# Kernel tuning notes

Hardware: AMD Instinct MI355X
Metric: run time of the kernel (lower is better)

Reference implementation:

```python
import jax, jax.numpy as jnp
import numpy as np


def _ctc_greedy_decode(probs, table, default_char):
    """Greedy CTC decode (tf.keras.backend.ctc_decode, greedy=True) + label->char lookup.

    probs: [B, T, C] post-softmax scores; blank index = C-1 (tf convention).
    Returns [B, T] int32 char codes, left-packed, padded positions -> default_char
    (tf pads the dense decoded tensor with -1; the hash-table lookup of -1 yields
    the table's default value).
    """
    B, T, C = probs.shape
    blank = C - 1
    best = jnp.argmax(probs, axis=-1).astype(jnp.int32)           # [B, T]
    # collapse repeats: keep first of each run
    prev = jnp.concatenate([jnp.full((B, 1), -1, jnp.int32), best[:, :-1]], axis=1)
    valid = (best != prev) & (best != blank)                      # [B, T]
    # left-pack valid labels via scatter (invalid entries routed to a dummy column T)
    pos = jnp.cumsum(valid.astype(jnp.int32), axis=1) - 1         # output slot per step
    scatter_col = jnp.where(valid, pos, T)
    out = jnp.full((B, T + 1), -1, jnp.int32)
    b_idx = jnp.arange(B)[:, None]
    out = out.at[b_idx, scatter_col].set(best)
    labels = out[:, :T]                                           # [B, T], -1 padded
    # hash-table lookup: valid labels -> chars, -1 padding -> default_value
    chars = jnp.where(labels >= 0,
                      table[jnp.clip(labels, 0, C - 1)],
                      jnp.int32(default_char))
    return chars


def setup_inputs() -> dict:
    key = jax.random.key(0)
    k1, k2 = jax.random.split(key)
    B, T, C = 1024, 512, 128
    inputs = jax.random.uniform(k1, (B, T, C), dtype=jnp.float32)
    table = jax.random.randint(k2, (C,), 0, 128, dtype=jnp.int32)
    return {"inputs": inputs, "table": table, "default_char": 32}


def reference(inputs, table, default_char):
    return _ctc_greedy_decode(inputs, table, default_char)
```

## Files before the change

### kernel.cpp

```cpp
#include <hip/hip_runtime.h>


constexpr int T_DIM = 512;
constexpr int C_DIM = 128;
constexpr int BLANK = C_DIM - 1;
constexpr int BLOCK = 512;
constexpr int TS_PER_ITER = BLOCK / 8;
constexpr int N_ITER = T_DIM / TS_PER_ITER;

__global__ __launch_bounds__(BLOCK, 4) void ctc_decode_kernel(
    const float* __restrict__ probs,
    const int* __restrict__ table,
    const int* __restrict__ defc_p,
    int* __restrict__ out)
{
    __shared__ int s_best[T_DIM];
    __shared__ int s_chars[T_DIM];
    __shared__ int s_table[C_DIM];
    __shared__ int s_wavesums[BLOCK / 64];

    const int b    = blockIdx.x;
    const int tid  = threadIdx.x;
    const int lane = tid & 63;
    const int wave = tid >> 6;

    if (tid < C_DIM) s_table[tid] = table[tid];
    const int defc = defc_p[0];

    const float* row = probs + (size_t)b * T_DIM * C_DIM;

    const int g = lane >> 3;
    const int h = lane & 7;

    float4 pf[4];
    {
        const float* p0 = row + (size_t)(wave * 8 + g) * C_DIM + h * 4;
        #pragma unroll
        for (int j = 0; j < 4; ++j) pf[j] = *(const float4*)(p0 + j * 32);
    }

    for (int it = 0; it < N_ITER; ++it) {
        float4 v[4];
        #pragma unroll
        for (int j = 0; j < 4; ++j) v[j] = pf[j];

        if (it + 1 < N_ITER) {
            const float* pn = row + (size_t)((it + 1) * TS_PER_ITER + wave * 8 + g) * C_DIM + h * 4;
            #pragma unroll
            for (int j = 0; j < 4; ++j) pf[j] = *(const float4*)(pn + j * 32);
        }

        float bv = -1.0f; int bi = 0;
        #pragma unroll
        for (int j = 0; j < 4; ++j) {
            const int i0 = j * 32 + h * 4;
            if (v[j].x > bv) { bv = v[j].x; bi = i0;     }
            if (v[j].y > bv) { bv = v[j].y; bi = i0 + 1; }
            if (v[j].z > bv) { bv = v[j].z; bi = i0 + 2; }
            if (v[j].w > bv) { bv = v[j].w; bi = i0 + 3; }
        }

        unsigned long long key =
            ((unsigned long long)__float_as_uint(bv) << 32) | (unsigned)(127 - bi);

        #pragma unroll
        for (int m = 1; m <= 4; m <<= 1) {
            const unsigned long long ok = __shfl_xor(key, m);
            if (ok > key) key = ok;
        }

        if (h == 0) s_best[it * TS_PER_ITER + wave * 8 + g] = 127 - (int)(key & 127u);
    }
    __syncthreads();

    const int best_t = s_best[tid];
    const int prev   = (tid > 0) ? s_best[tid - 1] : -1;
    const int valid  = (best_t != prev && best_t != BLANK) ? 1 : 0;

    int scan = valid;
    #pragma unroll
    for (int off = 1; off < 64; off <<= 1) {
        const int vv = __shfl_up(scan, off);
        if (lane >= off) scan += vv;
    }
    if (lane == 63) s_wavesums[wave] = scan;
    __syncthreads();
    if (tid == 0) {
        int acc = 0;
        #pragma unroll
        for (int w = 0; w < BLOCK / 64; ++w) {
            const int tmp = s_wavesums[w];
            s_wavesums[w] = acc;
            acc += tmp;
        }
    }
    __syncthreads();
    const int pos = scan + s_wavesums[wave] - 1;

    s_chars[tid] = defc;
    __syncthreads();
    if (valid) s_chars[pos] = s_table[best_t];
    __syncthreads();
    out[(size_t)b * T_DIM + tid] = s_chars[tid];
}

extern "C" void kernel_launch(void* const* d_in, const int* in_sizes, int n_in,
                              void* d_out, int out_size, void* d_ws, size_t ws_size,
                              hipStream_t stream) {
    const float* probs = (const float*)d_in[0];
    const int*   table = (const int*)d_in[1];
    const int*   defc  = (const int*)d_in[2];
    int*         out   = (int*)d_out;

    const int B = out_size / T_DIM;
    ctc_decode_kernel<<<dim3(B), dim3(BLOCK), 0, stream>>>(probs, table, defc, out);
}
```

Measured before the change: 355.7 us.

## Use 4 lanes per timestep with double-buffered 8-float4 prefetch

Each timestep's 128-class row is now reduced by 4 lanes instead of 8, so each lane loads eight float4s instead of four and each iteration covers twice as many timesteps. The loop is fully unrolled into four stages with two register buffers, which keeps up to two iterations of loads in flight. This raises memory-level parallelism and cuts shuffle steps. In exchange, register use per thread goes up, which may lower occupancy under the launch bounds.

```diff
diff --git a/kernel.cpp b/kernel.cpp
--- a/kernel.cpp
+++ b/kernel.cpp
@@ -5,8 +5,48 @@
 constexpr int C_DIM = 128;
 constexpr int BLANK = C_DIM - 1;
 constexpr int BLOCK = 512;
-constexpr int TS_PER_ITER = BLOCK / 8;
+constexpr int TS_PER_ITER = BLOCK / 4;
 constexpr int N_ITER = T_DIM / TS_PER_ITER;
+
+__device__ __forceinline__ void load8(float4 (&buf)[8], const float* p) {
+    #pragma unroll
+    for (int j = 0; j < 8; ++j) buf[j] = *(const float4*)(p + j * 16);
+}
+
+__device__ __forceinline__ void lane_argmax(const float4 (&buf)[8], int h,
+                                            float& bv, int& bi) {
+    float bvA = -1.0f; int biA = 0;
+    #pragma unroll
+    for (int j = 0; j < 4; ++j) {
+        const int i0 = 16 * j + 4 * h;
+        if (buf[j].x > bvA) { bvA = buf[j].x; biA = i0;     }
+        if (buf[j].y > bvA) { bvA = buf[j].y; biA = i0 + 1; }
+        if (buf[j].z > bvA) { bvA = buf[j].z; biA = i0 + 2; }
+        if (buf[j].w > bvA) { bvA = buf[j].w; biA = i0 + 3; }
+    }
+    float bvB = -1.0f; int biB = 64;
+    #pragma unroll
+    for (int j = 4; j < 8; ++j) {
+        const int i0 = 16 * j + 4 * h;
+        if (buf[j].x > bvB) { bvB = buf[j].x; biB = i0;     }
+        if (buf[j].y > bvB) { bvB = buf[j].y; biB = i0 + 1; }
+        if (buf[j].z > bvB) { bvB = buf[j].z; biB = i0 + 2; }
+        if (buf[j].w > bvB) { bvB = buf[j].w; biB = i0 + 3; }
+    }
+    if (bvB > bvA) { bvA = bvB; biA = biB; }
+    bv = bvA; bi = biA;
+}
+
+__device__ __forceinline__ int team_reduce(float bv, int bi) {
+    unsigned long long key =
+        ((unsigned long long)__float_as_uint(bv) << 32) | (unsigned)(127 - bi);
+    #pragma unroll
+    for (int m = 1; m <= 2; m <<= 1) {
+        const unsigned long long ok = __shfl_xor(key, m);
+        if (ok > key) key = ok;
+    }
+    return 127 - (int)(key & 127u);
+}
 
 __global__ __launch_bounds__(BLOCK, 4) void ctc_decode_kernel(
     const float* __restrict__ probs,
@@ -29,47 +69,40 @@
 
     const float* row = probs + (size_t)b * T_DIM * C_DIM;
 
-    const int g = lane >> 3;
-    const int h = lane & 7;
+    const int g = lane >> 2;
+    const int h = lane & 3;
 
-    float4 pf[4];
+    const int ts_local = wave * 16 + g;
+    const float* base  = row + (size_t)ts_local * C_DIM + h * 4;
+    const size_t step  = (size_t)TS_PER_ITER * C_DIM;
+
+    float4 bufA[8], bufB[8];
+    load8(bufA, base);
+    load8(bufB, base + step);
+
+    float bv; int bi;
+
+    lane_argmax(bufA, h, bv, bi);
+    load8(bufA, base + 2 * step);
     {
-        const float* p0 = row + (size_t)(wave * 8 + g) * C_DIM + h * 4;
-        #pragma unroll
-        for (int j = 0; j < 4; ++j) pf[j] = *(const float4*)(p0 + j * 32);
+        const int idx = team_reduce(bv, bi);
+        if (h == 0) s_best[0 * TS_PER_ITER + ts_local] = idx;
     }
-
-    for (int it = 0; it < N_ITER; ++it) {
-        float4 v[4];
-        #pragma unroll
-        for (int j = 0; j < 4; ++j) v[j] = pf[j];
-
-        if (it + 1 < N_ITER) {
-            const float* pn = row + (size_t)((it + 1) * TS_PER_ITER + wave * 8 + g) * C_DIM + h * 4;
-            #pragma unroll
-            for (int j = 0; j < 4; ++j) pf[j] = *(const float4*)(pn + j * 32);
-        }
-
-        float bv = -1.0f; int bi = 0;
-        #pragma unroll
-        for (int j = 0; j < 4; ++j) {
-            const int i0 = j * 32 + h * 4;
-            if (v[j].x > bv) { bv = v[j].x; bi = i0;     }
-            if (v[j].y > bv) { bv = v[j].y; bi = i0 + 1; }
-            if (v[j].z > bv) { bv = v[j].z; bi = i0 + 2; }
-            if (v[j].w > bv) { bv = v[j].w; bi = i0 + 3; }
-        }
-
-        unsigned long long key =
-            ((unsigned long long)__float_as_uint(bv) << 32) | (unsigned)(127 - bi);
-
-        #pragma unroll
-        for (int m = 1; m <= 4; m <<= 1) {
-            const unsigned long long ok = __shfl_xor(key, m);
-            if (ok > key) key = ok;
-        }
-
-        if (h == 0) s_best[it * TS_PER_ITER + wave * 8 + g] = 127 - (int)(key & 127u);
+    lane_argmax(bufB, h, bv, bi);
+    load8(bufB, base + 3 * step);
+    {
+        const int idx = team_reduce(bv, bi);
+        if (h == 0) s_best[1 * TS_PER_ITER + ts_local] = idx;
+    }
+    lane_argmax(bufA, h, bv, bi);
+    {
+        const int idx = team_reduce(bv, bi);
+        if (h == 0) s_best[2 * TS_PER_ITER + ts_local] = idx;
+    }
+    lane_argmax(bufB, h, bv, bi);
+    {
+        const int idx = team_reduce(bv, bi);
+        if (h == 0) s_best[3 * TS_PER_ITER + ts_local] = idx;
     }
     __syncthreads();
 
```

New measurement: 356.0 us. Within noise of the previous version (+0.1%).
